# Kernel optimization log

Hardware: AMD Instinct MI355X
Metric: run time of the kernel (lower is better)

The kernel has to match this reference:

```python
import jax, jax.numpy as jnp
import numpy as np

G_OFF = 1e-6
G_ON = 1e-4
K_V = 0.5
BATCH, SIZE_IN, SIZE_OUT = 512, 2048, 2048


def setup_inputs() -> dict:
    key = jax.random.key(0)
    k1, k2 = jax.random.split(key)
    stdv = 1.0 / np.sqrt(SIZE_IN)
    x = jax.random.normal(k1, (BATCH, SIZE_IN), dtype=jnp.float32)
    weights = jax.random.normal(k2, (SIZE_OUT, SIZE_IN), dtype=jnp.float32) * stdv
    bias = jnp.zeros((SIZE_OUT,), dtype=jnp.float32)
    return {"x": x, "weights": weights, "bias": bias}


def reference(x, weights, bias):
    # inputs with bias column of ones: (B, in+1)
    inputs = jnp.concatenate([x, jnp.ones((x.shape[0], 1), dtype=x.dtype)], axis=1)
    # weights_and_bias: (in+1, out)
    wb = jnp.concatenate([weights.T, bias[None, :]], axis=0)

    V = K_V * inputs                               # (B, in+1)
    max_wb = jnp.max(jnp.abs(wb))
    k_G = (G_ON - G_OFF) / max_wb
    k_I = K_V * k_G
    G_eff = k_G * wb
    G_pos = G_OFF + jnp.maximum(G_eff, 0.0)        # (in+1, out)
    G_neg = G_OFF - jnp.minimum(G_eff, 0.0)        # (in+1, out)

    # The torch code builds an interleaved G of shape (in+1, 2*out), computes
    # I_ind = V[:,:,None] * G[None,:,:], sums over the input axis, then takes
    # even - odd columns. That is exactly V @ G_pos - V @ G_neg.
    I_total = V @ G_pos - V @ G_neg                # (B, out)
    return I_total / k_I
```

## Files before the change

kernel.cpp:

```cpp
#include <hip/hip_runtime.h>
#include <hip/hip_bf16.h>


typedef float  float4_t __attribute__((ext_vector_type(4)));
typedef short  short8_t __attribute__((ext_vector_type(8)));
typedef float  floatx4  __attribute__((ext_vector_type(4)));

constexpr int M = 512, N = 2048, K = 2048;
constexpr int BM = 64, BN = 64, BK = 128;
constexpr int LDK = BK + 8;
constexpr int NT  = K / BK;

__global__ __launch_bounds__(512)
void memristor_gemm(const float* __restrict__ x, const float* __restrict__ w,
                    const float* __restrict__ bias, float* __restrict__ out)
{
    __shared__ __hip_bfloat16 As[2][BM][LDK];
    __shared__ __hip_bfloat16 Bs[2][BN][LDK];

    const int tid  = threadIdx.x;
    const int bn   = blockIdx.x, bm = blockIdx.y;
    const int lane = tid & 63;
    const int wave = tid >> 6;
    const int wsp  = wave & 3;
    const int kp   = wave >> 2;
    const int wm   = (wsp >> 1) * 32;
    const int wn   = (wsp & 1) * 32;
    const int l16  = lane & 15;
    const int quad = lane >> 4;

    const int srow = tid >> 5;
    const int sc4  = tid & 31;

    const float* xp = x + (size_t)(bm * BM + srow) * K + sc4 * 4;
    const float* wp = w + (size_t)(bn * BN + srow) * K + sc4 * 4;

    floatx4 acc[2][2];
    #pragma unroll
    for (int i = 0; i < 2; ++i)
        #pragma unroll
        for (int j = 0; j < 2; ++j)
            acc[i][j] = (floatx4){0.f, 0.f, 0.f, 0.f};

    float4_t va[4], vb[4];

    auto load_tile = [&](int t) {
        #pragma unroll
        for (int r = 0; r < 4; ++r) {
            va[r] = *(const float4_t*)(xp + (size_t)r * 16 * K + t * BK);
            vb[r] = *(const float4_t*)(wp + (size_t)r * 16 * K + t * BK);
        }
    };

    auto stage = [&](int buf) {
        #pragma unroll
        for (int r = 0; r < 4; ++r) {
            const int row = r * 16 + srow;
            union { __hip_bfloat16 h[4]; unsigned long long u; } ua, ub;
            ua.h[0] = __float2bfloat16(va[r].x);
            ua.h[1] = __float2bfloat16(va[r].y);
            ua.h[2] = __float2bfloat16(va[r].z);
            ua.h[3] = __float2bfloat16(va[r].w);
            ub.h[0] = __float2bfloat16(vb[r].x);
            ub.h[1] = __float2bfloat16(vb[r].y);
            ub.h[2] = __float2bfloat16(vb[r].z);
            ub.h[3] = __float2bfloat16(vb[r].w);
            *(unsigned long long*)&As[buf][row][sc4 * 4] = ua.u;
            *(unsigned long long*)&Bs[buf][row][sc4 * 4] = ub.u;
        }
    };

    auto compute = [&](int buf) {
        #pragma unroll
        for (int s = 0; s < 2; ++s) {
            const int kb = kp * 64 + s * 32 + quad * 8;
            short8_t af[2], bf[2];
            af[0] = *(const short8_t*)&As[buf][wm + l16][kb];
            af[1] = *(const short8_t*)&As[buf][wm + 16 + l16][kb];
            bf[0] = *(const short8_t*)&Bs[buf][wn + l16][kb];
            bf[1] = *(const short8_t*)&Bs[buf][wn + 16 + l16][kb];
            #pragma unroll
            for (int i = 0; i < 2; ++i)
                #pragma unroll
                for (int j = 0; j < 2; ++j)
                    acc[i][j] = __builtin_amdgcn_mfma_f32_16x16x32_bf16(
                        af[i], bf[j], acc[i][j], 0, 0, 0);
        }
    };

    load_tile(0);
    stage(0);
    load_tile(1);
    __syncthreads();

    for (int t = 0; t < NT; ++t) {
        const int cur = t & 1;
        compute(cur);
        if (t + 1 < NT) {
            stage(cur ^ 1);
            if (t + 2 < NT) load_tile(t + 2);
        }
        __syncthreads();
    }

    float* scrb = (float*)&As[0][0][0];
    if (kp == 1) {
        #pragma unroll
        for (int i = 0; i < 2; ++i)
            #pragma unroll
            for (int j = 0; j < 2; ++j) {
                float* p = scrb + ((wsp * 32 + j * 16 + l16) * 36 + i * 16 + quad * 4);
                *(floatx4*)p = acc[i][j];
            }
    }
    __syncthreads();
    if (kp == 0) {
        #pragma unroll
        for (int j = 0; j < 2; ++j) {
            const int col = bn * BN + wn + j * 16 + l16;
            const float bv = bias[col];
            #pragma unroll
            for (int i = 0; i < 2; ++i) {
                const floatx4 part = *(const floatx4*)(
                    scrb + ((wsp * 32 + j * 16 + l16) * 36 + i * 16 + quad * 4));
                const int row0 = bm * BM + wm + i * 16 + quad * 4;
                #pragma unroll
                for (int r = 0; r < 4; ++r)
                    out[(size_t)(row0 + r) * N + col] = acc[i][j][r] + part[r] + bv;
            }
        }
    }
}

extern "C" void kernel_launch(void* const* d_in, const int* in_sizes, int n_in,
                              void* d_out, int out_size, void* d_ws, size_t ws_size,
                              hipStream_t stream) {
    const float* x    = (const float*)d_in[0];
    const float* w    = (const float*)d_in[1];
    const float* bias = (const float*)d_in[2];
    float* out = (float*)d_out;

    dim3 grid(N / BN, M / BM);
    memristor_gemm<<<grid, 512, 0, stream>>>(x, w, bias, out);
}
```

Measured before the change: 81.70 us.

## Pre-convert inputs to bf16 and stream tiles via direct global-to-LDS loads

Adds a separate pass that converts x and weights to bf16 in workspace. The GEMM then loads tiles with global_load_lds straight into XOR-swizzled shared memory, through a three-stage buffer ring with explicit vmcnt waits. This removes the register-staged conversion from the main loop and halves the bytes the GEMM reads. In exchange it adds a full conversion pass that reads and writes the whole weight matrix every call, plus an extra kernel launch.

```diff
diff --git a/kernel.cpp b/kernel.cpp
--- a/kernel.cpp
+++ b/kernel.cpp
@@ -8,15 +8,44 @@
 
 constexpr int M = 512, N = 2048, K = 2048;
 constexpr int BM = 64, BN = 64, BK = 128;
-constexpr int LDK = BK + 8;
-constexpr int NT  = K / BK;
+constexpr int NT = K / BK;
+constexpr int XCHUNKS = M * K / 8;
+constexpr int WCHUNKS = N * K / 8;
+constexpr int BUFB = BM * BK * 2;
+
+__device__ __forceinline__ void gload16(const void* g, void* l) {
+    __builtin_amdgcn_global_load_lds(
+        (const __attribute__((address_space(1))) void*)g,
+        (__attribute__((address_space(3))) void*)l, 16, 0, 0);
+}
+
+__global__ __launch_bounds__(256)
+void convert_bf16(const float* __restrict__ x, const float* __restrict__ w,
+                  __hip_bfloat16* __restrict__ xb, __hip_bfloat16* __restrict__ wb)
+{
+    const int i = blockIdx.x * 256 + threadIdx.x;
+    const float* src;
+    __hip_bfloat16* dst;
+    size_t off;
+    if (i < XCHUNKS) { src = x; dst = xb; off = (size_t)i * 8; }
+    else             { src = w; dst = wb; off = (size_t)(i - XCHUNKS) * 8; }
+    const float4_t a = *(const float4_t*)(src + off);
+    const float4_t b = *(const float4_t*)(src + off + 4);
+    union { __hip_bfloat16 h[8]; short8_t s; } u;
+    u.h[0] = __float2bfloat16(a.x); u.h[1] = __float2bfloat16(a.y);
+    u.h[2] = __float2bfloat16(a.z); u.h[3] = __float2bfloat16(a.w);
+    u.h[4] = __float2bfloat16(b.x); u.h[5] = __float2bfloat16(b.y);
+    u.h[6] = __float2bfloat16(b.z); u.h[7] = __float2bfloat16(b.w);
+    *(short8_t*)(dst + off) = u.s;
+}
 
 __global__ __launch_bounds__(512)
-void memristor_gemm(const float* __restrict__ x, const float* __restrict__ w,
+void memristor_gemm(const __hip_bfloat16* __restrict__ xb,
+                    const __hip_bfloat16* __restrict__ wb,
                     const float* __restrict__ bias, float* __restrict__ out)
 {
-    __shared__ __hip_bfloat16 As[2][BM][LDK];
-    __shared__ __hip_bfloat16 Bs[2][BN][LDK];
+    __shared__ __hip_bfloat16 As[3][BM][BK];
+    __shared__ __hip_bfloat16 Bs[3][BN][BK];
 
     const int tid  = threadIdx.x;
     const int bn   = blockIdx.x, bm = blockIdx.y;
@@ -29,11 +58,24 @@
     const int l16  = lane & 15;
     const int quad = lane >> 4;
 
-    const int srow = tid >> 5;
-    const int sc4  = tid & 31;
+    const int srow0 = wave * 4 + (lane >> 4);
+    const int cl    = lane & 15;
+    const int gc    = (cl ^ (srow0 & 7)) * 8;
 
-    const float* xp = x + (size_t)(bm * BM + srow) * K + sc4 * 4;
-    const float* wp = w + (size_t)(bn * BN + srow) * K + sc4 * 4;
+    const __hip_bfloat16* ga0 = xb + (size_t)(bm * BM + srow0) * K + gc;
+    const __hip_bfloat16* ga1 = ga0 + (size_t)32 * K;
+    const __hip_bfloat16* gb0 = wb + (size_t)(bn * BN + srow0) * K + gc;
+    const __hip_bfloat16* gb1 = gb0 + (size_t)32 * K;
+
+    auto stage = [&](int t, int buf) {
+        const size_t go = (size_t)t * BK;
+        char* la = (char*)As + buf * BUFB + wave * 1024;
+        char* lb = (char*)Bs + buf * BUFB + wave * 1024;
+        gload16(ga0 + go, la);
+        gload16(ga1 + go, la + 8192);
+        gload16(gb0 + go, lb);
+        gload16(gb1 + go, lb + 8192);
+    };
 
     floatx4 acc[2][2];
     #pragma unroll
@@ -42,68 +84,52 @@
         for (int j = 0; j < 2; ++j)
             acc[i][j] = (floatx4){0.f, 0.f, 0.f, 0.f};
 
-    float4_t va[4], vb[4];
+    const int sw  = (l16 & 7) * 16;
+    const int ra0 = (wm + l16) * 256,      ra1 = ra0 + 16 * 256;
+    const int rb0 = (wn + l16) * 256,      rb1 = rb0 + 16 * 256;
 
-    auto load_tile = [&](int t) {
+    auto compute = [&](int buf) {
+        const char* ab = (const char*)As + buf * BUFB;
+        const char* bb = (const char*)Bs + buf * BUFB;
         #pragma unroll
-        for (int r = 0; r < 4; ++r) {
-            va[r] = *(const float4_t*)(xp + (size_t)r * 16 * K + t * BK);
-            vb[r] = *(const float4_t*)(wp + (size_t)r * 16 * K + t * BK);
+        for (int s = 0; s < 2; ++s) {
+            const int co = ((kp * 8 + s * 4 + quad) * 16) ^ sw;
+            const short8_t af0 = *(const short8_t*)(ab + ra0 + co);
+            const short8_t af1 = *(const short8_t*)(ab + ra1 + co);
+            const short8_t bf0 = *(const short8_t*)(bb + rb0 + co);
+            const short8_t bf1 = *(const short8_t*)(bb + rb1 + co);
+            acc[0][0] = __builtin_amdgcn_mfma_f32_16x16x32_bf16(af0, bf0, acc[0][0], 0, 0, 0);
+            acc[0][1] = __builtin_amdgcn_mfma_f32_16x16x32_bf16(af0, bf1, acc[0][1], 0, 0, 0);
+            acc[1][0] = __builtin_amdgcn_mfma_f32_16x16x32_bf16(af1, bf0, acc[1][0], 0, 0, 0);
+            acc[1][1] = __builtin_amdgcn_mfma_f32_16x16x32_bf16(af1, bf1, acc[1][1], 0, 0, 0);
         }
     };
 
-    auto stage = [&](int buf) {
-        #pragma unroll
-        for (int r = 0; r < 4; ++r) {
-            const int row = r * 16 + srow;
-            union { __hip_bfloat16 h[4]; unsigned long long u; } ua, ub;
-            ua.h[0] = __float2bfloat16(va[r].x);
-            ua.h[1] = __float2bfloat16(va[r].y);
-            ua.h[2] = __float2bfloat16(va[r].z);
-            ua.h[3] = __float2bfloat16(va[r].w);
-            ub.h[0] = __float2bfloat16(vb[r].x);
-            ub.h[1] = __float2bfloat16(vb[r].y);
-            ub.h[2] = __float2bfloat16(vb[r].z);
-            ub.h[3] = __float2bfloat16(vb[r].w);
-            *(unsigned long long*)&As[buf][row][sc4 * 4] = ua.u;
-            *(unsigned long long*)&Bs[buf][row][sc4 * 4] = ub.u;
-        }
-    };
+    stage(0, 0);
+    stage(1, 1);
+    asm volatile("s_waitcnt vmcnt(4)" ::: "memory");
+    __builtin_amdgcn_s_barrier();
+    asm volatile("" ::: "memory");
 
-    auto compute = [&](int buf) {
-        #pragma unroll
-        for (int s = 0; s < 2; ++s) {
-            const int kb = kp * 64 + s * 32 + quad * 8;
-            short8_t af[2], bf[2];
-            af[0] = *(const short8_t*)&As[buf][wm + l16][kb];
-            af[1] = *(const short8_t*)&As[buf][wm + 16 + l16][kb];
-            bf[0] = *(const short8_t*)&Bs[buf][wn + l16][kb];
-            bf[1] = *(const short8_t*)&Bs[buf][wn + 16 + l16][kb];
-            #pragma unroll
-            for (int i = 0; i < 2; ++i)
-                #pragma unroll
-                for (int j = 0; j < 2; ++j)
-                    acc[i][j] = __builtin_amdgcn_mfma_f32_16x16x32_bf16(
-                        af[i], bf[j], acc[i][j], 0, 0, 0);
-        }
-    };
-
-    load_tile(0);
-    stage(0);
-    load_tile(1);
+    int cb = 0, sb = 2;
+    for (int t = 0; t < NT - 2; ++t) {
+        stage(t + 2, sb);
+        compute(cb);
+        asm volatile("s_waitcnt vmcnt(4)" ::: "memory");
+        __builtin_amdgcn_s_barrier();
+        asm volatile("" ::: "memory");
+        cb = (cb == 2) ? 0 : cb + 1;
+        sb = (sb == 2) ? 0 : sb + 1;
+    }
+    compute(cb);
+    asm volatile("s_waitcnt vmcnt(0)" ::: "memory");
+    __builtin_amdgcn_s_barrier();
+    asm volatile("" ::: "memory");
+    cb = (cb == 2) ? 0 : cb + 1;
+    compute(cb);
     __syncthreads();
 
-    for (int t = 0; t < NT; ++t) {
-        const int cur = t & 1;
-        compute(cur);
-        if (t + 1 < NT) {
-            stage(cur ^ 1);
-            if (t + 2 < NT) load_tile(t + 2);
-        }
-        __syncthreads();
-    }
-
-    float* scrb = (float*)&As[0][0][0];
+    float* scrb = (float*)As;
     if (kp == 1) {
         #pragma unroll
         for (int i = 0; i < 2; ++i)
@@ -140,6 +166,11 @@
     const float* bias = (const float*)d_in[2];
     float* out = (float*)d_out;
 
+    __hip_bfloat16* xbf = (__hip_bfloat16*)d_ws;
+    __hip_bfloat16* wbf = xbf + (size_t)M * K;
+
+    convert_bf16<<<(XCHUNKS + WCHUNKS) / 256, 256, 0, stream>>>(x, w, xbf, wbf);
+
     dim3 grid(N / BN, M / BM);
-    memristor_gemm<<<grid, 512, 0, stream>>>(x, w, bias, out);
+    memristor_gemm<<<grid, 512, 0, stream>>>(xbf, wbf, bias, out);
 }
```

Measured after the change: 82.54 us. About the same (+1.0%).
